# Optimization experiments

Hardware: AMD Instinct MI355X
Metric: run time of the kernel (lower is better)

## Reference

```python
import jax, jax.numpy as jnp
import numpy as np

BS, N, H, W = 32, 8, 512, 512

def setup_inputs() -> dict:
    key = jax.random.key(0)
    k1, k2, k3 = jax.random.split(key, 3)
    pred_iou = jax.random.uniform(k1, (BS, N), dtype=jnp.float32)
    target_masks = jax.random.randint(k2, (BS, H, W), 0, 2, dtype=jnp.int32)
    pred_masks = jax.random.uniform(k3, (BS, N, H, W), dtype=jnp.float32)
    return {"pred_iou": pred_iou, "target_masks": target_masks, "pred_masks": pred_masks}

def reference(pred_iou, target_masks, pred_masks):
    # Binary Jaccard (torchmetrics): threshold preds at 0.5, target > 0.
    pred_bin = pred_masks > 0.5                      # [bs, n, H, W]
    tgt_bin = (target_masks > 0)[:, None, :, :]      # [bs, 1, H, W] broadcast over n
    inter = jnp.sum(pred_bin & tgt_bin, axis=(-2, -1)).astype(jnp.float32)  # [bs, n]
    union = jnp.sum(pred_bin | tgt_bin, axis=(-2, -1)).astype(jnp.float32)  # [bs, n]
    actual_iou = jnp.where(union > 0, inter / jnp.maximum(union, 1.0), 0.0)  # [bs, n]
    squared_error = (pred_iou - actual_iou) ** 2
    return squared_error
```

## Files before the change

### kernel.cpp

```cpp
#include <hip/hip_runtime.h>


#define BS      32
#define NMASKS  8
#define HW      (512 * 512)
#define WPI     (HW / 256)
#define TOTAL_W (BS * WPI)
#define GROUPS  8
#define SPAN    (HW / GROUPS)
#define BLOCK   256
#define NPAIRS  (BS * NMASKS)
#define ITERS   (SPAN / (BLOCK * 4))

typedef int   iv4 __attribute__((ext_vector_type(4)));
typedef float fv4 __attribute__((ext_vector_type(4)));

__global__ __launch_bounds__(BLOCK) void build_bitmask(
    const int* __restrict__ tgt,
    unsigned long long* __restrict__ bm)
{
    const int lane  = threadIdx.x & 63;
    const int gwave = blockIdx.x * (BLOCK / 64) + (threadIdx.x >> 6);
    const int w0    = gwave * (TOTAL_W / 1024);

#pragma unroll 4
    for (int i = 0; i < TOTAL_W / 1024; ++i) {
        const int w = w0 + i;
        const iv4 t4 = __builtin_nontemporal_load(
            (const iv4*)(tgt + (size_t)w * 256 + (size_t)lane * 4));
        const unsigned long long b0 = __ballot(t4.x > 0);
        const unsigned long long b1 = __ballot(t4.y > 0);
        const unsigned long long b2 = __ballot(t4.z > 0);
        const unsigned long long b3 = __ballot(t4.w > 0);
        if (lane == 0) {
            unsigned long long* p = bm + (size_t)w * 4;
            p[0] = b0; p[1] = b1; p[2] = b2; p[3] = b3;
        }
    }
}

__global__ __launch_bounds__(BLOCK, 8) void iou_count_kernel(
    const float* __restrict__ pred,
    const unsigned long long* __restrict__ bm,
    unsigned long long* __restrict__ ws)
{
    const int idx = blockIdx.x;
    const int b   = idx >> 6;
    const int n   = (idx >> 3) & 7;
    const int grp = idx & 7;
    const int tid = threadIdx.x;
    const int wv  = tid >> 6;

    const float* pbase =
        pred + ((size_t)(b * NMASKS + n)) * HW + (size_t)grp * SPAN + (size_t)tid * 4;

    const int wbase = __builtin_amdgcn_readfirstlane(
        b * WPI + grp * (SPAN / 256) + wv);

    unsigned int inter = 0u, uni = 0u;

#pragma unroll 4
    for (int it = 0; it < ITERS; ++it) {
        const fv4 p4 = __builtin_nontemporal_load(
            (const fv4*)(pbase + (size_t)it * (BLOCK * 4)));

        const unsigned long long* wp = bm + (size_t)(wbase + it * 4) * 4;
        const unsigned long long w0 = wp[0], w1 = wp[1], w2 = wp[2], w3 = wp[3];

        const unsigned long long p0 = __ballot(p4.x > 0.5f);
        const unsigned long long p1 = __ballot(p4.y > 0.5f);
        const unsigned long long p2 = __ballot(p4.z > 0.5f);
        const unsigned long long p3 = __ballot(p4.w > 0.5f);

        inter += (unsigned)(__popcll(p0 & w0) + __popcll(p1 & w1) +
                            __popcll(p2 & w2) + __popcll(p3 & w3));
        uni   += (unsigned)(__popcll(p0 | w0) + __popcll(p1 | w1) +
                            __popcll(p2 | w2) + __popcll(p3 | w3));
    }

    __shared__ unsigned long long s[BLOCK / 64];
    if ((tid & 63) == 0)
        s[wv] = ((unsigned long long)inter << 32) | (unsigned long long)uni;
    __syncthreads();

    if (tid == 0)
        ws[(size_t)grp * NPAIRS + (size_t)b * NMASKS + n] =
            s[0] + s[1] + s[2] + s[3];
}

__global__ __launch_bounds__(NPAIRS) void finalize_kernel(
    const float* __restrict__ pred_iou,
    const unsigned long long* __restrict__ ws,
    float* __restrict__ out)
{
    const int i = threadIdx.x;
    unsigned long long v = 0ull;
#pragma unroll
    for (int g = 0; g < GROUPS; ++g)
        v += ws[(size_t)g * NPAIRS + i];

    const unsigned int inter = (unsigned int)(v >> 32);
    const unsigned int uni   = (unsigned int)(v & 0xffffffffu);
    const float iou = (uni > 0u) ? ((float)inter / (float)uni) : 0.0f;
    const float d = pred_iou[i] - iou;
    out[i] = d * d;
}

extern "C" void kernel_launch(void* const* d_in, const int* in_sizes, int n_in,
                              void* d_out, int out_size, void* d_ws, size_t ws_size,
                              hipStream_t stream) {
    const float* pred_iou = (const float*)d_in[0];
    const int*   tgt      = (const int*)d_in[1];
    const float* pred     = (const float*)d_in[2];
    float* out = (float*)d_out;

    unsigned long long* partials = (unsigned long long*)d_ws;
    unsigned long long* bm = (unsigned long long*)((char*)d_ws + (64 << 10));

    build_bitmask<<<1024 / (BLOCK / 64), BLOCK, 0, stream>>>(tgt, bm);
    iou_count_kernel<<<BS * NMASKS * GROUPS, BLOCK, 0, stream>>>(pred, bm, partials);
    finalize_kernel<<<1, NPAIRS, 0, stream>>>(pred_iou, partials, out);
}
```

Measured before the change: 367.3 us.

## Stage target bitmask in LDS and double-buffer prediction loads in groups

Each block now copies its slice of the target bitmask into shared memory once, and the main loop reads it from LDS instead of from global memory on every iteration. Prediction loads are issued in groups of eight float4 into two register buffers, so the next group is in flight while the current one is counted. The launch-bounds occupancy hint drops from 8 to 4 to leave room for the extra registers. The cost is more register pressure and lower occupancy, and the kernel is already bandwidth-bound, so the gain may be small.

```diff
diff --git a/kernel.cpp b/kernel.cpp
--- a/kernel.cpp
+++ b/kernel.cpp
@@ -8,16 +8,21 @@
 #define TOTAL_W (BS * WPI)
 #define GROUPS  8
 #define SPAN    (HW / GROUPS)
+#define WPB     (SPAN / 256)
 #define BLOCK   256
 #define NPAIRS  (BS * NMASKS)
 #define ITERS   (SPAN / (BLOCK * 4))
+#define PG      8
+#define NGRP    (ITERS / PG)
 
-typedef int   iv4 __attribute__((ext_vector_type(4)));
-typedef float fv4 __attribute__((ext_vector_type(4)));
+typedef int    iv4 __attribute__((ext_vector_type(4)));
+typedef float  fv4 __attribute__((ext_vector_type(4)));
+typedef unsigned long long u64;
+typedef u64    uv2 __attribute__((ext_vector_type(2)));
 
 __global__ __launch_bounds__(BLOCK) void build_bitmask(
     const int* __restrict__ tgt,
-    unsigned long long* __restrict__ bm)
+    u64* __restrict__ bm)
 {
     const int lane  = threadIdx.x & 63;
     const int gwave = blockIdx.x * (BLOCK / 64) + (threadIdx.x >> 6);
@@ -28,21 +33,21 @@
         const int w = w0 + i;
         const iv4 t4 = __builtin_nontemporal_load(
             (const iv4*)(tgt + (size_t)w * 256 + (size_t)lane * 4));
-        const unsigned long long b0 = __ballot(t4.x > 0);
-        const unsigned long long b1 = __ballot(t4.y > 0);
-        const unsigned long long b2 = __ballot(t4.z > 0);
-        const unsigned long long b3 = __ballot(t4.w > 0);
+        const u64 b0 = __ballot(t4.x > 0);
+        const u64 b1 = __ballot(t4.y > 0);
+        const u64 b2 = __ballot(t4.z > 0);
+        const u64 b3 = __ballot(t4.w > 0);
         if (lane == 0) {
-            unsigned long long* p = bm + (size_t)w * 4;
+            u64* p = bm + (size_t)w * 4;
             p[0] = b0; p[1] = b1; p[2] = b2; p[3] = b3;
         }
     }
 }
 
-__global__ __launch_bounds__(BLOCK, 8) void iou_count_kernel(
+__global__ __launch_bounds__(BLOCK, 4) void iou_count_kernel(
     const float* __restrict__ pred,
-    const unsigned long long* __restrict__ bm,
-    unsigned long long* __restrict__ ws)
+    const u64* __restrict__ bm,
+    u64* __restrict__ ws)
 {
     const int idx = blockIdx.x;
     const int b   = idx >> 6;
@@ -51,36 +56,61 @@
     const int tid = threadIdx.x;
     const int wv  = tid >> 6;
 
+    __shared__ u64 sbm[WPB * 4];
+    {
+        const size_t slice = ((size_t)b * WPI + (size_t)grp * WPB) * 4;
+        *(uv2*)(sbm + 2 * tid) = *(const uv2*)(bm + slice + 2 * tid);
+    }
+    __syncthreads();
+
     const float* pbase =
         pred + ((size_t)(b * NMASKS + n)) * HW + (size_t)grp * SPAN + (size_t)tid * 4;
 
-    const int wbase = __builtin_amdgcn_readfirstlane(
-        b * WPI + grp * (SPAN / 256) + wv);
-
     unsigned int inter = 0u, uni = 0u;
 
-#pragma unroll 4
-    for (int it = 0; it < ITERS; ++it) {
-        const fv4 p4 = __builtin_nontemporal_load(
-            (const fv4*)(pbase + (size_t)it * (BLOCK * 4)));
+    fv4 buf[2][PG];
 
-        const unsigned long long* wp = bm + (size_t)(wbase + it * 4) * 4;
-        const unsigned long long w0 = wp[0], w1 = wp[1], w2 = wp[2], w3 = wp[3];
+#pragma unroll
+    for (int j = 0; j < PG; ++j)
+        buf[0][j] = __builtin_nontemporal_load(
+            (const fv4*)(pbase + (size_t)j * (BLOCK * 4)));
 
-        const unsigned long long p0 = __ballot(p4.x > 0.5f);
-        const unsigned long long p1 = __ballot(p4.y > 0.5f);
-        const unsigned long long p2 = __ballot(p4.z > 0.5f);
-        const unsigned long long p3 = __ballot(p4.w > 0.5f);
+    for (int g = 0; g < NGRP; ++g) {
+        const int cur = g & 1;
+        const int nxt = cur ^ 1;
 
-        inter += (unsigned)(__popcll(p0 & w0) + __popcll(p1 & w1) +
-                            __popcll(p2 & w2) + __popcll(p3 & w3));
-        uni   += (unsigned)(__popcll(p0 | w0) + __popcll(p1 | w1) +
-                            __popcll(p2 | w2) + __popcll(p3 | w3));
+        if (g + 1 < NGRP) {
+#pragma unroll
+            for (int j = 0; j < PG; ++j)
+                buf[nxt][j] = __builtin_nontemporal_load(
+                    (const fv4*)(pbase + (size_t)((g + 1) * PG + j) * (BLOCK * 4)));
+        }
+
+#pragma unroll
+        for (int j = 0; j < PG; ++j) {
+            const int it = g * PG + j;
+            const int wl = it * 4 + wv;
+            const u64 w0 = sbm[wl * 4 + 0];
+            const u64 w1 = sbm[wl * 4 + 1];
+            const u64 w2 = sbm[wl * 4 + 2];
+            const u64 w3 = sbm[wl * 4 + 3];
+
+            const fv4 p4 = buf[cur][j];
+            const u64 p0 = __ballot(p4.x > 0.5f);
+            const u64 p1 = __ballot(p4.y > 0.5f);
+            const u64 p2 = __ballot(p4.z > 0.5f);
+            const u64 p3 = __ballot(p4.w > 0.5f);
+
+            inter += (unsigned)(__popcll(p0 & w0) + __popcll(p1 & w1) +
+                                __popcll(p2 & w2) + __popcll(p3 & w3));
+            uni   += (unsigned)(__popcll(p0 | w0) + __popcll(p1 | w1) +
+                                __popcll(p2 | w2) + __popcll(p3 | w3));
+        }
     }
 
-    __shared__ unsigned long long s[BLOCK / 64];
+    __shared__ u64 s[BLOCK / 64];
     if ((tid & 63) == 0)
-        s[wv] = ((unsigned long long)inter << 32) | (unsigned long long)uni;
+        s[wv] = ((u64)inter << 32) | (u64)uni;
     __syncthreads();
 
     if (tid == 0)
@@ -90,11 +120,11 @@
 
 __global__ __launch_bounds__(NPAIRS) void finalize_kernel(
     const float* __restrict__ pred_iou,
-    const unsigned long long* __restrict__ ws,
+    const u64* __restrict__ ws,
     float* __restrict__ out)
 {
     const int i = threadIdx.x;
-    unsigned long long v = 0ull;
+    u64 v = 0ull;
 #pragma unroll
     for (int g = 0; g < GROUPS; ++g)
         v += ws[(size_t)g * NPAIRS + i];
@@ -114,8 +144,8 @@
     const float* pred     = (const float*)d_in[2];
     float* out = (float*)d_out;
 
-    unsigned long long* partials = (unsigned long long*)d_ws;
-    unsigned long long* bm = (unsigned long long*)((char*)d_ws + (64 << 10));
+    u64* partials = (u64*)d_ws;
+    u64* bm = (u64*)((char*)d_ws + (64 << 10));
 
     build_bitmask<<<1024 / (BLOCK / 64), BLOCK, 0, stream>>>(tgt, bm);
     iou_count_kernel<<<BS * NMASKS * GROUPS, BLOCK, 0, stream>>>(pred, bm, partials);
```

Result: slower. 391.2 us (+6.5%).
